# Optimization experiments

Hardware: AMD Instinct MI355X
Metric: run time of the kernel (lower is better)

The kernel has to match this reference:

```python
import jax, jax.numpy as jnp
import numpy as np

NTOKENS = 8192
H = 1024
FFN = 2048
NEXPERTS = 64
TOPK = 2
M = NTOKENS * TOPK  # total routed slots


def setup_inputs() -> dict:
    key = jax.random.key(0)
    k1, k2, k3 = jax.random.split(key, 3)
    inputs_shard = jax.random.normal(k1, (NTOKENS, H), dtype=jnp.float32)
    w1 = jax.random.normal(k2, (NEXPERTS, H, FFN), dtype=jnp.float32) * 0.02
    w2 = jax.random.normal(k3, (NEXPERTS, FFN, H), dtype=jnp.float32) * 0.02
    # Balanced routing: each expert receives exactly M // NEXPERTS slots.
    rng = np.random.default_rng(0)
    per_expert = M // NEXPERTS
    eid_flat = rng.permutation(np.repeat(np.arange(M // per_expert), per_expert))  # [M] expert id per (token,k)
    order = np.argsort(eid_flat, kind='stable')  # slot -> flat (token,k) index
    scatter_flat = np.empty(M, dtype=np.int64)
    scatter_flat[order] = np.arange(M)  # (token,k) -> slot in expert-sorted buffer
    scatter_index = jnp.asarray(scatter_flat.reshape(NTOKENS, TOPK))
    splits = jnp.full((NEXPERTS,), per_expert, dtype=jnp.int64)
    return {"inputs_shard": inputs_shard, "w1": w1, "w2": w2,
            "scatter_index": scatter_index, "splits": splits}


def reference(inputs_shard, w1, w2, scatter_index, splits):
    ntokens, topk = scatter_index.shape
    m = ntokens * topk
    nexperts = w1.shape[0]
    per_expert = m // nexperts  # splits are balanced by construction
    # AG-scatter: place each token copy into its expert-sorted slot.
    slot_to_tk = jnp.argsort(scatter_index.reshape(-1))  # slot -> (token,k) flat idx
    token = slot_to_tk // topk                            # slot -> source token
    expanded = inputs_shard[token]                        # [M, H]
    # Grouped GEMM 1 (h -> ffn) + exact gelu, per expert block.
    xg = expanded.reshape(nexperts, per_expert, -1)       # [G, M/G, H]
    h1 = jnp.einsum('geh,ghf->gef', xg, w1)               # [G, M/G, FFN]
    a = jax.nn.gelu(h1, approximate=False)
    # Grouped GEMM 2 (ffn -> h).
    h2 = jnp.einsum('gef,gfh->geh', a, w2).reshape(m, -1)  # [M, H]
    # Gather-RS: gather topk partials per token and reduce (sum).
    out = h2[scatter_index.reshape(-1)].reshape(ntokens, topk, -1).sum(axis=1)
    return out
```

## Files before the change

### kernel.cpp

```cpp
#include <hip/hip_runtime.h>
#include <hip/hip_bf16.h>
#include <math.h>

#define NTOK 8192
#define HD   1024
#define FFND 2048
#define NE   64
#define MTOT 16384
#define PER_E 256

typedef __attribute__((ext_vector_type(8))) short bh8;
typedef __attribute__((ext_vector_type(4))) float f4;
typedef unsigned short u16;
typedef unsigned int   u32;

__device__ __forceinline__ u16 f2bf(float f) {
  union { float f; u32 u; } x; x.f = f;
  u32 r = x.u + 0x7fffu + ((x.u >> 16) & 1u);
  return (u16)(r >> 16);
}

__device__ __forceinline__ u32 pk2(float lo, float hi) {
  __hip_bfloat162 h = __float22bfloat162_rn(make_float2(lo, hi));
  union { __hip_bfloat162 h; u32 u; } c; c.h = h;
  return c.u;
}

__global__ void k_build_s2t(const int* __restrict__ sidx, int* __restrict__ s2t) {
  int i = blockIdx.x * 256 + threadIdx.x;
  s2t[sidx[i]] = i >> 1;
}

__global__ void k_gather_x(const float* __restrict__ inp, const int* __restrict__ s2t,
                           u16* __restrict__ X) {
  int idx = blockIdx.x * 256 + threadIdx.x;
  int slot = idx >> 7;
  int c    = idx & 127;
  const float* src = inp + (size_t)s2t[slot] * HD + c * 8;
  float v[8];
  *(f4*)(v)     = *(const f4*)(src);
  *(f4*)(v + 4) = *(const f4*)(src + 4);
  u32 o[4];
  #pragma unroll
  for (int j = 0; j < 4; ++j) o[j] = pk2(v[2 * j], v[2 * j + 1]);
  *(uint4*)(X + (size_t)slot * HD + c * 8) = *(uint4*)o;
}

template<int K, int N, bool GELU>
__global__ __launch_bounds__(512, 4)
void moe_gemm(const u16* __restrict__ Abf, const float* __restrict__ Bf,
              u16* __restrict__ actout, float* __restrict__ redout)
{
  constexpr int BM = 256, BN = 128, BK = 64;
  constexpr int NB = N / BN;
  constexpr int NT = K / BK;
  constexpr int ABYTES = BM * 128;
  __shared__ __align__(16) char lds[2 * ABYTES + BN * 128];
  char* Bs = lds + 2 * ABYTES;

  const int d = blockIdx.y * NB + blockIdx.x;
  const int x = d & 7, j = d >> 3;
  const int e  = x * (NE / 8) + j / NB;
  const int n0 = (j % NB) * BN;
  const int row0 = e * PER_E;
  const int tid  = threadIdx.x;
  const int lane = tid & 63, wid = tid >> 6;
  const int wr   = wid >> 1, wc = wid & 1;

  const u16*   Arow = Abf + (size_t)row0 * K;
  const float* Bsrc = Bf + (size_t)e * K * N + n0;

  auto stageA = [&](int buf, int k0) {
    char* dst = lds + buf * ABYTES;
    #pragma unroll
    for (int i = 0; i < 4; ++i) {
      int c = i * 512 + tid;
      int r = c >> 3, kc = c & 7;
      int kswz = kc ^ (r & 7);
      __builtin_amdgcn_global_load_lds(
          (const void*)(Arow + (size_t)r * K + k0 + kswz * 8),
          (void*)(dst + c * 16), 16, 0, 0);
    }
  };
  auto loadB = [&](float* br, int k0) {
    #pragma unroll
    for (int i = 0; i < 2; ++i) {
      int c = i * 512 + tid;
      int n = c & 127, kc = c >> 7;
      const float* p = Bsrc + (size_t)(k0 + kc * 8) * N + n;
      #pragma unroll
      for (int jj = 0; jj < 8; ++jj) br[i * 8 + jj] = p[(size_t)jj * N];
    }
  };
  auto writeB = [&](const float* br) {
    #pragma unroll
    for (int i = 0; i < 2; ++i) {
      int c = i * 512 + tid;
      int n = c & 127, kc = c >> 7;
      u32 q[4];
      #pragma unroll
      for (int jj = 0; jj < 4; ++jj) q[jj] = pk2(br[i * 8 + 2 * jj], br[i * 8 + 2 * jj + 1]);
      *(uint4*)(Bs + n * 128 + ((kc * 16) ^ ((n & 7) << 4))) = *(uint4*)q;
    }
  };

  f4 acc[4][4] = {};
  float breg[16];

  stageA(0, 0);
  loadB(breg, 0);
  writeB(breg);
  asm volatile("s_waitcnt vmcnt(0) lgkmcnt(0)" ::: "memory");
  __builtin_amdgcn_sched_barrier(0);
  __builtin_amdgcn_s_barrier();
  __builtin_amdgcn_sched_barrier(0);

  int cur = 0;
  for (int t = 0; t < NT; ++t) {
    const char* As = lds + cur * ABYTES;
    if (t + 1 < NT) {
      stageA(cur ^ 1, (t + 1) * BK);
      loadB(breg, (t + 1) * BK);
    }
    __builtin_amdgcn_s_setprio(1);
    #pragma unroll
    for (int kk = 0; kk < 2; ++kk) {
      int kByte = kk * 64 + ((lane >> 4) << 4);
      bh8 a[4], b[4];
      #pragma unroll
      for (int m = 0; m < 4; ++m) {
        int r = wr * 64 + m * 16 + (lane & 15);
        a[m] = *(const bh8*)(As + r * 128 + (kByte ^ ((r & 7) << 4)));
      }
      #pragma unroll
      for (int n = 0; n < 4; ++n) {
        int r = wc * 64 + n * 16 + (lane & 15);
        b[n] = *(const bh8*)(Bs + r * 128 + (kByte ^ ((r & 7) << 4)));
      }
      #pragma unroll
      for (int m = 0; m < 4; ++m)
        #pragma unroll
        for (int n = 0; n < 4; ++n)
          acc[m][n] = __builtin_amdgcn_mfma_f32_16x16x32_bf16(a[m], b[n], acc[m][n], 0, 0, 0);
    }
    __builtin_amdgcn_s_setprio(0);
    __builtin_amdgcn_s_barrier();
    __builtin_amdgcn_sched_barrier(0);
    if (t + 1 < NT) {
      writeB(breg);
      asm volatile("s_waitcnt vmcnt(0) lgkmcnt(0)" ::: "memory");
      __builtin_amdgcn_sched_barrier(0);
      __builtin_amdgcn_s_barrier();
      __builtin_amdgcn_sched_barrier(0);
      cur ^= 1;
    }
  }

  #pragma unroll
  for (int m = 0; m < 4; ++m) {
    #pragma unroll
    for (int n = 0; n < 4; ++n) {
      int rowb = wr * 64 + m * 16 + ((lane >> 4) << 2);
      int col  = n0 + wc * 64 + n * 16 + (lane & 15);
      #pragma unroll
      for (int jj = 0; jj < 4; ++jj) {
        float xv = acc[m][n][jj];
        if (GELU) {
          float y = fminf(fmaxf(xv, -8.f), 8.f);
          float u = 0.7978845608f * (y + 0.044715f * y * y * y);
          float t2 = __expf(-2.f * u);
          float g = __fdividef(y, 1.f + t2);
          actout[(size_t)(row0 + rowb + jj) * N + col] = f2bf(g);
        } else {
          redout[(size_t)(row0 + rowb + jj) * N + col] = xv;
        }
      }
    }
  }
}

__global__ void k_reduce(const float* __restrict__ h2, const int* __restrict__ sidx,
                         float* __restrict__ out) {
  int t = blockIdx.x;
  int c = threadIdx.x;
  const f4* r0 = (const f4*)(h2 + (size_t)sidx[2 * t] * HD);
  const f4* r1 = (const f4*)(h2 + (size_t)sidx[2 * t + 1] * HD);
  ((f4*)(out + (size_t)t * HD))[c] = r0[c] + r1[c];
}

extern "C" void kernel_launch(void* const* d_in, const int* in_sizes, int n_in,
                              void* d_out, int out_size, void* d_ws, size_t ws_size,
                              hipStream_t stream) {
  const float* inp  = (const float*)d_in[0];
  const float* w1   = (const float*)d_in[1];
  const float* w2   = (const float*)d_in[2];
  const int*   sidx = (const int*)d_in[3];
  float* out = (float*)d_out;

  char* ws   = (char*)d_ws;
  int*   s2t = (int*)ws;
  u16*   X   = (u16*)(ws + (1 << 20));
  u16*   act = (u16*)(ws + (1 << 20) + (32u << 20));
  float* h2  = (float*)(ws + (1 << 20) + (96u << 20));

  k_build_s2t<<<MTOT / 256, 256, 0, stream>>>(sidx, s2t);
  k_gather_x<<<(MTOT * (HD / 8)) / 256, 256, 0, stream>>>(inp, s2t, X);
  moe_gemm<HD, FFND, true><<<dim3(FFND / 128, NE), 512, 0, stream>>>(X, w1, act, nullptr);
  moe_gemm<FFND, HD, false><<<dim3(HD / 128, NE), 512, 0, stream>>>(act, w2, nullptr, h2);
  k_reduce<<<NTOK, 256, 0, stream>>>(h2, sidx, out);
}
```

Before: 308.8 us.

## Narrow GEMM2 tile width and store second GEMM output as bf16

Makes the GEMM tile width a template parameter and launches the second grouped GEMM with 64-column tiles, doubling its block count to improve occupancy and load balance. The second GEMM output is now written as bf16 instead of fp32, and the reduce kernel converts back, halving intermediate write and read traffic. The narrower tile halves A-tile reuse in GEMM2, and the bf16 intermediate adds rounding error before the top-k sum.

Result: no change. 314.0 us (+1.7%).

```diff
diff --git a/kernel.cpp b/kernel.cpp
--- a/kernel.cpp
+++ b/kernel.cpp
@@ -18,6 +18,10 @@
   union { float f; u32 u; } x; x.f = f;
   u32 r = x.u + 0x7fffu + ((x.u >> 16) & 1u);
   return (u16)(r >> 16);
+}
+
+__device__ __forceinline__ float bf2f(u16 b) {
+  union { u32 u; float f; } x; x.u = ((u32)b) << 16; return x.f;
 }
 
 __device__ __forceinline__ u32 pk2(float lo, float hi) {
@@ -46,14 +50,16 @@
   *(uint4*)(X + (size_t)slot * HD + c * 8) = *(uint4*)o;
 }
 
-template<int K, int N, bool GELU>
+template<int K, int N, int BN, bool GELU>
 __global__ __launch_bounds__(512, 4)
 void moe_gemm(const u16* __restrict__ Abf, const float* __restrict__ Bf,
-              u16* __restrict__ actout, float* __restrict__ redout)
+              u16* __restrict__ outp)
 {
-  constexpr int BM = 256, BN = 128, BK = 64;
+  constexpr int BM = 256, BK = 64;
   constexpr int NB = N / BN;
   constexpr int NT = K / BK;
+  constexpr int NF = BN / 32;
+  constexpr int BITER = BN / 64;
   constexpr int ABYTES = BM * 128;
   __shared__ __align__(16) char lds[2 * ABYTES + BN * 128];
   char* Bs = lds + 2 * ABYTES;
@@ -84,9 +90,9 @@
   };
   auto loadB = [&](float* br, int k0) {
     #pragma unroll
-    for (int i = 0; i < 2; ++i) {
+    for (int i = 0; i < BITER; ++i) {
       int c = i * 512 + tid;
-      int n = c & 127, kc = c >> 7;
+      int n = c & (BN - 1), kc = c / BN;
       const float* p = Bsrc + (size_t)(k0 + kc * 8) * N + n;
       #pragma unroll
       for (int jj = 0; jj < 8; ++jj) br[i * 8 + jj] = p[(size_t)jj * N];
@@ -94,9 +100,9 @@
   };
   auto writeB = [&](const float* br) {
     #pragma unroll
-    for (int i = 0; i < 2; ++i) {
+    for (int i = 0; i < BITER; ++i) {
       int c = i * 512 + tid;
-      int n = c & 127, kc = c >> 7;
+      int n = c & (BN - 1), kc = c / BN;
       u32 q[4];
       #pragma unroll
       for (int jj = 0; jj < 4; ++jj) q[jj] = pk2(br[i * 8 + 2 * jj], br[i * 8 + 2 * jj + 1]);
@@ -104,8 +110,8 @@
     }
   };
 
-  f4 acc[4][4] = {};
-  float breg[16];
+  f4 acc[4][NF] = {};
+  float breg[BITER * 8];
 
   stageA(0, 0);
   loadB(breg, 0);
@@ -126,21 +132,21 @@
     #pragma unroll
     for (int kk = 0; kk < 2; ++kk) {
       int kByte = kk * 64 + ((lane >> 4) << 4);
-      bh8 a[4], b[4];
+      bh8 a[4], b[NF];
       #pragma unroll
       for (int m = 0; m < 4; ++m) {
         int r = wr * 64 + m * 16 + (lane & 15);
         a[m] = *(const bh8*)(As + r * 128 + (kByte ^ ((r & 7) << 4)));
       }
       #pragma unroll
-      for (int n = 0; n < 4; ++n) {
-        int r = wc * 64 + n * 16 + (lane & 15);
+      for (int n = 0; n < NF; ++n) {
+        int r = wc * (NF * 16) + n * 16 + (lane & 15);
         b[n] = *(const bh8*)(Bs + r * 128 + (kByte ^ ((r & 7) << 4)));
       }
       #pragma unroll
       for (int m = 0; m < 4; ++m)
         #pragma unroll
-        for (int n = 0; n < 4; ++n)
+        for (int n = 0; n < NF; ++n)
           acc[m][n] = __builtin_amdgcn_mfma_f32_16x16x32_bf16(a[m], b[n], acc[m][n], 0, 0, 0);
     }
     __builtin_amdgcn_s_setprio(0);
@@ -159,9 +165,9 @@
   #pragma unroll
   for (int m = 0; m < 4; ++m) {
     #pragma unroll
-    for (int n = 0; n < 4; ++n) {
+    for (int n = 0; n < NF; ++n) {
       int rowb = wr * 64 + m * 16 + ((lane >> 4) << 2);
-      int col  = n0 + wc * 64 + n * 16 + (lane & 15);
+      int col  = n0 + wc * (NF * 16) + n * 16 + (lane & 15);
       #pragma unroll
       for (int jj = 0; jj < 4; ++jj) {
         float xv = acc[m][n][jj];
@@ -170,22 +176,28 @@
           float u = 0.7978845608f * (y + 0.044715f * y * y * y);
           float t2 = __expf(-2.f * u);
           float g = __fdividef(y, 1.f + t2);
-          actout[(size_t)(row0 + rowb + jj) * N + col] = f2bf(g);
+          outp[(size_t)(row0 + rowb + jj) * N + col] = f2bf(g);
         } else {
-          redout[(size_t)(row0 + rowb + jj) * N + col] = xv;
+          outp[(size_t)(row0 + rowb + jj) * N + col] = f2bf(xv);
         }
       }
     }
   }
 }
 
-__global__ void k_reduce(const float* __restrict__ h2, const int* __restrict__ sidx,
+__global__ void k_reduce(const u16* __restrict__ h2, const int* __restrict__ sidx,
                          float* __restrict__ out) {
   int t = blockIdx.x;
   int c = threadIdx.x;
-  const f4* r0 = (const f4*)(h2 + (size_t)sidx[2 * t] * HD);
-  const f4* r1 = (const f4*)(h2 + (size_t)sidx[2 * t + 1] * HD);
-  ((f4*)(out + (size_t)t * HD))[c] = r0[c] + r1[c];
+  const u16* r0 = h2 + (size_t)sidx[2 * t] * HD + c * 4;
+  const u16* r1 = h2 + (size_t)sidx[2 * t + 1] * HD + c * 4;
+  u16 a0[4], a1[4];
+  *(uint2*)a0 = *(const uint2*)r0;
+  *(uint2*)a1 = *(const uint2*)r1;
+  f4 s;
+  #pragma unroll
+  for (int jj = 0; jj < 4; ++jj) s[jj] = bf2f(a0[jj]) + bf2f(a1[jj]);
+  *(f4*)(out + (size_t)t * HD + c * 4) = s;
 }
 
 extern "C" void kernel_launch(void* const* d_in, const int* in_sizes, int n_in,
@@ -201,11 +213,11 @@
   int*   s2t = (int*)ws;
   u16*   X   = (u16*)(ws + (1 << 20));
   u16*   act = (u16*)(ws + (1 << 20) + (32u << 20));
-  float* h2  = (float*)(ws + (1 << 20) + (96u << 20));
+  u16*   h2  = (u16*)(ws + (1 << 20) + (96u << 20));
 
   k_build_s2t<<<MTOT / 256, 256, 0, stream>>>(sidx, s2t);
   k_gather_x<<<(MTOT * (HD / 8)) / 256, 256, 0, stream>>>(inp, s2t, X);
-  moe_gemm<HD, FFND, true><<<dim3(FFND / 128, NE), 512, 0, stream>>>(X, w1, act, nullptr);
-  moe_gemm<FFND, HD, false><<<dim3(HD / 128, NE), 512, 0, stream>>>(act, w2, nullptr, h2);
+  moe_gemm<HD, FFND, 128, true><<<dim3(FFND / 128, NE), 512, 0, stream>>>(X, w1, act);
+  moe_gemm<FFND, HD, 64, false><<<dim3(HD / 64, NE), 512, 0, stream>>>(act, w2, h2);
   k_reduce<<<NTOK, 256, 0, stream>>>(h2, sidx, out);
 }
```

## Issue B loads before A staging with partial vmcnt waits; store h2 as bf16

Applied to the files above, without the earlier changes.

The GEMM prologue and main loop now issue the weight (B) global loads before the A global_load_lds staging. Partial s_waitcnt vmcnt counts let writeB proceed once the B loads land, without draining the A prefetch, so the A copy overlaps the MFMA work and the LDS write of B. The second GEMM's output h2 is also stored as bf16 instead of fp32, halving its write traffic and the reduce kernel's read traffic, at the cost of extra rounding in the partial sums. The hand-counted vmcnt values depend on the exact number of loads each thread issues, so any change to the load pattern could break correctness.

Result: faster. 302.3 us (-2.1%).

```diff
diff --git a/kernel.cpp b/kernel.cpp
--- a/kernel.cpp
+++ b/kernel.cpp
@@ -18,6 +18,10 @@
   union { float f; u32 u; } x; x.f = f;
   u32 r = x.u + 0x7fffu + ((x.u >> 16) & 1u);
   return (u16)(r >> 16);
+}
+
+__device__ __forceinline__ float bf2f(u16 b) {
+  union { u32 u; float f; } x; x.u = ((u32)b) << 16; return x.f;
 }
 
 __device__ __forceinline__ u32 pk2(float lo, float hi) {
@@ -49,7 +53,7 @@
 template<int K, int N, bool GELU>
 __global__ __launch_bounds__(512, 4)
 void moe_gemm(const u16* __restrict__ Abf, const float* __restrict__ Bf,
-              u16* __restrict__ actout, float* __restrict__ redout)
+              u16* __restrict__ outp)
 {
   constexpr int BM = 256, BN = 128, BK = 64;
   constexpr int NB = N / BN;
@@ -107,10 +111,13 @@
   f4 acc[4][4] = {};
   float breg[16];
 
+  loadB(breg, 0);
+  __builtin_amdgcn_sched_barrier(0);
   stageA(0, 0);
-  loadB(breg, 0);
+  asm volatile("s_waitcnt vmcnt(4)" ::: "memory");
+  __builtin_amdgcn_sched_barrier(0);
   writeB(breg);
-  asm volatile("s_waitcnt vmcnt(0) lgkmcnt(0)" ::: "memory");
+  asm volatile("s_waitcnt lgkmcnt(0)" ::: "memory");
   __builtin_amdgcn_sched_barrier(0);
   __builtin_amdgcn_s_barrier();
   __builtin_amdgcn_sched_barrier(0);
@@ -119,9 +126,14 @@
   for (int t = 0; t < NT; ++t) {
     const char* As = lds + cur * ABYTES;
     if (t + 1 < NT) {
+      loadB(breg, (t + 1) * BK);
+      __builtin_amdgcn_sched_barrier(0);
       stageA(cur ^ 1, (t + 1) * BK);
-      loadB(breg, (t + 1) * BK);
-    }
+      asm volatile("s_waitcnt vmcnt(20)" ::: "memory");
+    } else {
+      asm volatile("s_waitcnt vmcnt(0)" ::: "memory");
+    }
+    __builtin_amdgcn_sched_barrier(0);
     __builtin_amdgcn_s_setprio(1);
     #pragma unroll
     for (int kk = 0; kk < 2; ++kk) {
@@ -147,8 +159,10 @@
     __builtin_amdgcn_s_barrier();
     __builtin_amdgcn_sched_barrier(0);
     if (t + 1 < NT) {
+      asm volatile("s_waitcnt vmcnt(4)" ::: "memory");
+      __builtin_amdgcn_sched_barrier(0);
       writeB(breg);
-      asm volatile("s_waitcnt vmcnt(0) lgkmcnt(0)" ::: "memory");
+      asm volatile("s_waitcnt lgkmcnt(0)" ::: "memory");
       __builtin_amdgcn_sched_barrier(0);
       __builtin_amdgcn_s_barrier();
       __builtin_amdgcn_sched_barrier(0);
@@ -170,22 +184,28 @@
           float u = 0.7978845608f * (y + 0.044715f * y * y * y);
           float t2 = __expf(-2.f * u);
           float g = __fdividef(y, 1.f + t2);
-          actout[(size_t)(row0 + rowb + jj) * N + col] = f2bf(g);
+          outp[(size_t)(row0 + rowb + jj) * N + col] = f2bf(g);
         } else {
-          redout[(size_t)(row0 + rowb + jj) * N + col] = xv;
+          outp[(size_t)(row0 + rowb + jj) * N + col] = f2bf(xv);
         }
       }
     }
   }
 }
 
-__global__ void k_reduce(const float* __restrict__ h2, const int* __restrict__ sidx,
+__global__ void k_reduce(const u16* __restrict__ h2, const int* __restrict__ sidx,
                          float* __restrict__ out) {
   int t = blockIdx.x;
   int c = threadIdx.x;
-  const f4* r0 = (const f4*)(h2 + (size_t)sidx[2 * t] * HD);
-  const f4* r1 = (const f4*)(h2 + (size_t)sidx[2 * t + 1] * HD);
-  ((f4*)(out + (size_t)t * HD))[c] = r0[c] + r1[c];
+  const u16* r0 = h2 + (size_t)sidx[2 * t] * HD + c * 4;
+  const u16* r1 = h2 + (size_t)sidx[2 * t + 1] * HD + c * 4;
+  u16 a0[4], a1[4];
+  *(uint2*)a0 = *(const uint2*)r0;
+  *(uint2*)a1 = *(const uint2*)r1;
+  f4 s;
+  #pragma unroll
+  for (int jj = 0; jj < 4; ++jj) s[jj] = bf2f(a0[jj]) + bf2f(a1[jj]);
+  *(f4*)(out + (size_t)t * HD + c * 4) = s;
 }
 
 extern "C" void kernel_launch(void* const* d_in, const int* in_sizes, int n_in,
@@ -201,11 +221,11 @@
   int*   s2t = (int*)ws;
   u16*   X   = (u16*)(ws + (1 << 20));
   u16*   act = (u16*)(ws + (1 << 20) + (32u << 20));
-  float* h2  = (float*)(ws + (1 << 20) + (96u << 20));
+  u16*   h2  = (u16*)(ws + (1 << 20) + (96u << 20));
 
   k_build_s2t<<<MTOT / 256, 256, 0, stream>>>(sidx, s2t);
   k_gather_x<<<(MTOT * (HD / 8)) / 256, 256, 0, stream>>>(inp, s2t, X);
-  moe_gemm<HD, FFND, true><<<dim3(FFND / 128, NE), 512, 0, stream>>>(X, w1, act, nullptr);
-  moe_gemm<FFND, HD, false><<<dim3(HD / 128, NE), 512, 0, stream>>>(act, w2, nullptr, h2);
+  moe_gemm<HD, FFND, true><<<dim3(FFND / 128, NE), 512, 0, stream>>>(X, w1, act);
+  moe_gemm<FFND, HD, false><<<dim3(HD / 128, NE), 512, 0, stream>>>(act, w2, h2);
   k_reduce<<<NTOK, 256, 0, stream>>>(h2, sidx, out);
 }
```
